# Kernel optimization log

Measured on AMD Instinct MI355X. Metric: run time of the kernel, lower is better.

## Reference

```python
import jax, jax.numpy as jnp
import numpy as np

QLEN, MLEN, BSZ = 1024, 1024, 8
D_MODEL, N_HEAD, D_HEAD = 512, 8, 64
KLEN = QLEN + MLEN
TAU = 1.0


def _rel_shift(x):
    # x: [qlen, klen, bsz, n_head] -- Transformer-XL relative shift
    q, k, b, n = x.shape
    zero_pad = jnp.zeros((q, 1, b, n), dtype=x.dtype)
    x_padded = jnp.concatenate([zero_pad, x], axis=1).reshape(k + 1, q, b, n)
    return x_padded[1:].reshape(q, k, b, n)


def setup_inputs() -> dict:
    key = jax.random.key(0)
    ks = jax.random.split(key, 8)
    w = jax.random.normal(ks[0], (QLEN, BSZ, D_MODEL), dtype=jnp.float32)
    r = jax.random.normal(ks[1], (KLEN, D_MODEL), dtype=jnp.float32)
    r_w_bias = jax.random.normal(ks[2], (N_HEAD, D_HEAD), dtype=jnp.float32) * 0.02
    r_r_bias = jax.random.normal(ks[3], (N_HEAD, D_HEAD), dtype=jnp.float32) * 0.02
    mems = jax.random.normal(ks[4], (MLEN, BSZ, D_MODEL), dtype=jnp.float32)
    W_qkv = jax.random.normal(ks[5], (D_MODEL, 3 * N_HEAD * D_HEAD), dtype=jnp.float32) * 0.02
    W_r = jax.random.normal(ks[6], (D_MODEL, N_HEAD * D_HEAD), dtype=jnp.float32) * 0.02
    W_o = jax.random.normal(ks[7], (N_HEAD * D_HEAD, D_MODEL), dtype=jnp.float32) * 0.02
    # causal mask with memory: query i can attend keys j <= i + MLEN
    i = jnp.arange(QLEN)[:, None]
    j = jnp.arange(KLEN)[None, :]
    attn_mask = (j > i + MLEN)[:, :, None]  # [qlen, klen, 1] bool, True = masked
    return {"w": w, "r": r, "r_w_bias": r_w_bias, "r_r_bias": r_r_bias,
            "mems": mems, "attn_mask": attn_mask,
            "W_qkv": W_qkv, "W_r": W_r, "W_o": W_o}


def reference(w, r, r_w_bias, r_r_bias, mems, attn_mask, W_qkv, W_r, W_o):
    qlen, bsz, d_model = w.shape
    n_head, d_head = r_w_bias.shape
    scale = 1.0 / np.sqrt(d_head).astype(np.float32)

    cat = jnp.concatenate([mems, w], axis=0)          # [klen, bsz, d_model]
    w_heads = cat @ W_qkv                              # [klen, bsz, 3*n*d]
    w_head_q, w_head_k, w_head_v = jnp.split(w_heads, 3, axis=-1)
    klen = w_head_k.shape[0]
    w_head_q = w_head_q[-qlen:].reshape(qlen, bsz, n_head, d_head)
    w_head_k = w_head_k.reshape(klen, bsz, n_head, d_head)
    w_head_v = w_head_v.reshape(klen, bsz, n_head, d_head)
    r_head_k = (r @ W_r).reshape(-1, n_head, d_head)   # [rlen, n, d]

    AC = jnp.einsum('ibnd,jbnd->ijbn', w_head_q + r_w_bias, w_head_k)
    BD = jnp.einsum('ibnd,jnd->ijbn', w_head_q + r_r_bias, r_head_k)
    BD = _rel_shift(BD)

    attn_score = (AC + BD) * scale                     # [q, k, b, n]
    mask4 = attn_mask[:, :, :, None]                   # [q, k, 1, 1]
    attn_score = jnp.where(mask4, -jnp.inf, attn_score)
    attn_prob = jax.nn.softmax(attn_score * TAU, axis=1)

    # attention entropy per head (no-grad in original)
    p_safe = jnp.where(mask4, 1.0, attn_prob)
    temp = -attn_prob * jnp.log(p_safe)
    attn_entropy = jax.lax.stop_gradient(jnp.mean(jnp.sum(temp, axis=1), axis=(0, 1)))  # [n_head]

    attn_vec = jnp.einsum('ijbn,jbnd->ibnd', attn_prob, w_head_v)
    attn_vec = attn_vec.reshape(qlen, bsz, n_head * d_head)
    attn_out = attn_vec @ W_o                          # [q, b, d_model]
    return attn_out, attn_entropy
```

## Files before the change

### kernel.cpp

```cpp
#include <hip/hip_runtime.h>
#include <hip/hip_bf16.h>


#define QLEN 1024
#define MLEN 1024
#define KLEN 2048
#define BSZ 8
#define DMODEL 512
#define NHEAD 8
#define DHEAD 64
#define SCALE 0.125f
#define RPAD 2176
#define RTHR 8.0f

#define B_QW   0u
#define B_QR   8388608u
#define B_K    16777216u
#define B_VT   33554432u
#define B_R    50331648u
#define B_AVB  52559872u
#define B_ENT  60948480u
#define B_ABF  60952576u
#define B_WQT  77729792u
#define B_RBF  79302656u
#define B_WRT  81399808u
#define B_WOT  81924096u

typedef short bf16x8 __attribute__((ext_vector_type(8)));
typedef float f32x4  __attribute__((ext_vector_type(4)));

#define SWZ(row, byte) ((((row) << 7) + (((((byte) >> 4) ^ ((row) & 7)) << 4)) + ((byte) & 15)))

__device__ __forceinline__ unsigned short f2bf(float f) {
    union { float f; unsigned int u; } v; v.f = f;
    unsigned int r = v.u + 0x7FFFu + ((v.u >> 16) & 1u);
    return (unsigned short)(r >> 16);
}

__global__ __launch_bounds__(256) void cvt_cat(const float* __restrict__ mems,
                                               const float* __restrict__ w,
                                               unsigned short* __restrict__ Abf) {
    size_t e = ((size_t)blockIdx.x * 256 + threadIdx.x) * 8;
    int m = (int)(e >> 9), k = (int)(e & 511);
    int t = m >> 3, b = m & 7;
    const float* src = (t < MLEN) ? mems + ((size_t)t * 8 + b) * 512 + k
                                  : w    + ((size_t)(t - MLEN) * 8 + b) * 512 + k;
    float4 v0 = *reinterpret_cast<const float4*>(src);
    float4 v1 = *reinterpret_cast<const float4*>(src + 4);
    ushort4 o0, o1;
    o0.x = f2bf(v0.x); o0.y = f2bf(v0.y); o0.z = f2bf(v0.z); o0.w = f2bf(v0.w);
    o1.x = f2bf(v1.x); o1.y = f2bf(v1.y); o1.z = f2bf(v1.z); o1.w = f2bf(v1.w);
    *reinterpret_cast<ushort4*>(Abf + e)     = o0;
    *reinterpret_cast<ushort4*>(Abf + e + 4) = o1;
}

__global__ __launch_bounds__(256) void cvt_r(const float* __restrict__ r,
                                             unsigned short* __restrict__ rbf) {
    size_t e = ((size_t)blockIdx.x * 256 + threadIdx.x) * 8;
    float4 v0 = *reinterpret_cast<const float4*>(r + e);
    float4 v1 = *reinterpret_cast<const float4*>(r + e + 4);
    ushort4 o0, o1;
    o0.x = f2bf(v0.x); o0.y = f2bf(v0.y); o0.z = f2bf(v0.z); o0.w = f2bf(v0.w);
    o1.x = f2bf(v1.x); o1.y = f2bf(v1.y); o1.z = f2bf(v1.z); o1.w = f2bf(v1.w);
    *reinterpret_cast<ushort4*>(rbf + e)     = o0;
    *reinterpret_cast<ushort4*>(rbf + e + 4) = o1;
}

__global__ __launch_bounds__(256) void tcvt(const float* __restrict__ S,
                                            unsigned short* __restrict__ D,
                                            int R, int C) {
    __shared__ float t[32][33];
    int bx = blockIdx.x * 32;
    int by = blockIdx.y * 32;
    int x = threadIdx.x & 31, y = threadIdx.x >> 5;
    #pragma unroll
    for (int q = 0; q < 4; ++q)
        t[y + q * 8][x] = S[(size_t)(by + y + q * 8) * C + bx + x];
    __syncthreads();
    #pragma unroll
    for (int q = 0; q < 4; ++q)
        D[(size_t)(bx + y + q * 8) * R + by + x] = f2bf(t[x][y + q * 8]);
}

__global__ void zpad_r(unsigned short* __restrict__ Rg) {
    int idx = blockIdx.x * 256 + threadIdx.x;
    int n = idx >> 10, o = idx & 1023;
    uint4 z = make_uint4(0, 0, 0, 0);
    *reinterpret_cast<uint4*>(Rg + ((size_t)n * RPAD + KLEN) * 64 + o * 8) = z;
}

template<int MODE>
__global__ __launch_bounds__(256) void gemm_mfma(const unsigned short* __restrict__ A,
                                                 const unsigned short* __restrict__ Bt,
                                                 const float* __restrict__ rwb,
                                                 const float* __restrict__ rrb,
                                                 unsigned short* __restrict__ QW,
                                                 unsigned short* __restrict__ QR,
                                                 unsigned short* __restrict__ Kg,
                                                 unsigned short* __restrict__ VT,
                                                 unsigned short* __restrict__ Rg,
                                                 float* __restrict__ Cout) {
    __shared__ unsigned short Als[128][72];
    __shared__ unsigned short Bls[128][72];
    const int tid = threadIdx.x;
    const int wv = tid >> 6, lane = tid & 63, lg = lane >> 4, lc = lane & 15;
    const int wr = wv >> 1, wc = wv & 1;
    const int n0 = blockIdx.x * 128;
    const int m0 = blockIdx.y * 128;

    f32x4 acc[4][4];
    #pragma unroll
    for (int mi = 0; mi < 4; ++mi)
        #pragma unroll
        for (int ni = 0; ni < 4; ++ni)
            acc[mi][ni] = (f32x4){0.f, 0.f, 0.f, 0.f};

    for (int k0 = 0; k0 < 512; k0 += 64) {
        __syncthreads();
        #pragma unroll
        for (int q = 0; q < 4; ++q) {
            int c = q * 256 + tid;
            int row = c >> 3, off = (c & 7) * 8;
            *reinterpret_cast<uint4*>(&Als[row][off]) =
                *reinterpret_cast<const uint4*>(A + (size_t)(m0 + row) * 512 + k0 + off);
            *reinterpret_cast<uint4*>(&Bls[row][off]) =
                *reinterpret_cast<const uint4*>(Bt + (size_t)(n0 + row) * 512 + k0 + off);
        }
        __syncthreads();
        #pragma unroll
        for (int kk = 0; kk < 2; ++kk) {
            bf16x8 af[4], bfr[4];
            #pragma unroll
            for (int mi = 0; mi < 4; ++mi)
                af[mi] = *reinterpret_cast<const bf16x8*>(&Als[64 * wr + 16 * mi + lc][32 * kk + lg * 8]);
            #pragma unroll
            for (int ni = 0; ni < 4; ++ni)
                bfr[ni] = *reinterpret_cast<const bf16x8*>(&Bls[64 * wc + 16 * ni + lc][32 * kk + lg * 8]);
            #pragma unroll
            for (int mi = 0; mi < 4; ++mi)
                #pragma unroll
                for (int ni = 0; ni < 4; ++ni)
                    acc[mi][ni] = __builtin_amdgcn_mfma_f32_16x16x32_bf16(af[mi], bfr[ni], acc[mi][ni], 0, 0, 0);
        }
    }

    #pragma unroll
    for (int mi = 0; mi < 4; ++mi) {
        #pragma unroll
        for (int ni = 0; ni < 4; ++ni) {
            const int n = n0 + 64 * wc + 16 * ni + lc;
            float bw = 0.f, br = 0.f;
            int region = 0, hn = 0, d = 0;
            if (MODE == 0) {
                region = n >> 9; int cr = n & 511; hn = cr >> 6; d = cr & 63;
                if (region == 0) { bw = rwb[hn * 64 + d]; br = rrb[hn * 64 + d]; }
            }
            #pragma unroll
            for (int reg = 0; reg < 4; ++reg) {
                const int m = m0 + 64 * wr + 16 * mi + lg * 4 + reg;
                const float val = acc[mi][ni][reg];
                if (MODE == 0) {
                    int t = m >> 3, b = m & 7, bn = b * 8 + hn;
                    if (region == 0) {
                        if (t >= MLEN) {
                            size_t base = ((size_t)bn * QLEN + (t - MLEN)) * 64 + d;
                            QW[base] = f2bf(val + bw);
                            QR[base] = f2bf(val + br);
                        }
                    } else if (region == 1) {
                        Kg[((size_t)bn * KLEN + t) * 64 + d] = f2bf(val);
                    } else {
                        VT[((size_t)bn * 64 + d) * KLEN + t] = f2bf(val);
                    }
                } else if (MODE == 1) {
                    Rg[((size_t)(n >> 6) * RPAD + m) * 64 + (n & 63)] = f2bf(val);
                } else {
                    Cout[(size_t)m * 512 + n] = val;
                }
            }
        }
    }
}

__global__ __launch_bounds__(256, 3) void attn_mfma(const unsigned short* __restrict__ QWg,
                                                    const unsigned short* __restrict__ QRg,
                                                    const unsigned short* __restrict__ Kg,
                                                    const unsigned short* __restrict__ VTg,
                                                    const unsigned short* __restrict__ Rg,
                                                    unsigned short* __restrict__ AVB,
                                                    float* __restrict__ ENT) {
    __shared__ __attribute__((aligned(16))) unsigned short Klds[64 * 64];
    __shared__ __attribute__((aligned(16))) unsigned short Rblds[128 * 64];
    __shared__ __attribute__((aligned(16))) unsigned short Vtlds[64 * 64];
    __shared__ __attribute__((aligned(16))) unsigned short Plds[64 * 64];

    const int tid = threadIdx.x;
    const int w = tid >> 6, lane = tid & 63, lg = lane >> 4, lc = lane & 15;
    const int iblk = ((blockIdx.y >> 4) & 1) ? (15 - blockIdx.x) : blockIdx.x;
    const int i0 = iblk * 64;
    const int bn = blockIdx.y, b = bn >> 3, n = bn & 7;
    const int srow = tid >> 3;
    const int sch  = tid & 7;

    {
        const unsigned short* qwsrc = QWg + ((size_t)bn * QLEN + i0) * 64;
        const unsigned short* qrsrc = QRg + ((size_t)bn * QLEN + i0) * 64;
        #pragma unroll
        for (int q = 0; q < 2; ++q) {
            int row = srow + q * 32;
            *reinterpret_cast<uint4*>((char*)Klds + SWZ(row, sch * 16)) =
                *reinterpret_cast<const uint4*>(qwsrc + (size_t)row * 64 + sch * 8);
            *reinterpret_cast<uint4*>((char*)Rblds + SWZ(row, sch * 16)) =
                *reinterpret_cast<const uint4*>(qrsrc + (size_t)row * 64 + sch * 8);
        }
    }
    __syncthreads();
    bf16x8 aqw[2], aqr[2];
    #pragma unroll
    for (int k = 0; k < 2; ++k) {
        aqw[k] = *reinterpret_cast<const bf16x8*>((const char*)Klds + SWZ(16 * w + lc, 64 * k + 16 * lg));
        aqr[k] = *reinterpret_cast<const bf16x8*>((const char*)Rblds + SWZ(16 * w + lc, 64 * k + 16 * lg));
    }

    f32x4 Ofr[4];
    #pragma unroll
    for (int t = 0; t < 4; ++t) Ofr[t] = (f32x4){0.f, 0.f, 0.f, 0.f};
    float mreg[4] = {-1e30f, -1e30f, -1e30f, -1e30f};
    float lpart[4] = {0.f, 0.f, 0.f, 0.f};
    float tpart[4] = {0.f, 0.f, 0.f, 0.f};

    const int nj = iblk + 17;
    const unsigned short* kbase = Kg  + (size_t)bn * KLEN * 64;
    const unsigned short* vbase = VTg + (size_t)bn * 64 * KLEN;
    const unsigned short* rbase = Rg  + (size_t)n * RPAD * 64 + (size_t)(960 - i0) * 64;

    uint4 kr0, kr1, vr0, vr1, rr0, rr1, rr2, rr3;
    kr0 = *reinterpret_cast<const uint4*>(kbase + (size_t)(srow)      * 64 + sch * 8);
    kr1 = *reinterpret_cast<const uint4*>(kbase + (size_t)(srow + 32) * 64 + sch * 8);
    vr0 = *reinterpret_cast<const uint4*>(vbase + (size_t)(srow)      * KLEN + sch * 8);
    vr1 = *reinterpret_cast<const uint4*>(vbase + (size_t)(srow + 32) * KLEN + sch * 8);
    rr0 = *reinterpret_cast<const uint4*>(rbase + (size_t)(srow)      * 64 + sch * 8);
    rr1 = *reinterpret_cast<const uint4*>(rbase + (size_t)(srow + 32) * 64 + sch * 8);
    rr2 = *reinterpret_cast<const uint4*>(rbase + (size_t)(srow + 64) * 64 + sch * 8);
    rr3 = *reinterpret_cast<const uint4*>(rbase + (size_t)(srow + 96) * 64 + sch * 8);

    for (int jt = 0; jt < nj; ++jt) {
        const int j0 = jt * 64;
        __syncthreads();

        *reinterpret_cast<uint4*>((char*)Klds  + SWZ(srow,      sch * 16)) = kr0;
        *reinterpret_cast<uint4*>((char*)Klds  + SWZ(srow + 32, sch * 16)) = kr1;
        *reinterpret_cast<uint4*>((char*)Vtlds + SWZ(srow,      sch * 16)) = vr0;
        *reinterpret_cast<uint4*>((char*)Vtlds + SWZ(srow + 32, sch * 16)) = vr1;
        *reinterpret_cast<uint4*>((char*)Rblds + SWZ(srow,      sch * 16)) = rr0;
        *reinterpret_cast<uint4*>((char*)Rblds + SWZ(srow + 32, sch * 16)) = rr1;
        *reinterpret_cast<uint4*>((char*)Rblds + SWZ(srow + 64, sch * 16)) = rr2;
        *reinterpret_cast<uint4*>((char*)Rblds + SWZ(srow + 96, sch * 16)) = rr3;

        if (jt + 1 < nj) {
            const int j1 = j0 + 64;
            kr0 = *reinterpret_cast<const uint4*>(kbase + (size_t)(j1 + srow)      * 64 + sch * 8);
            kr1 = *reinterpret_cast<const uint4*>(kbase + (size_t)(j1 + srow + 32) * 64 + sch * 8);
            vr0 = *reinterpret_cast<const uint4*>(vbase + (size_t)(srow)      * KLEN + j1 + sch * 8);
            vr1 = *reinterpret_cast<const uint4*>(vbase + (size_t)(srow + 32) * KLEN + j1 + sch * 8);
            rr0 = *reinterpret_cast<const uint4*>(rbase + (size_t)(j1 + srow)      * 64 + sch * 8);
            rr1 = *reinterpret_cast<const uint4*>(rbase + (size_t)(j1 + srow + 32) * 64 + sch * 8);
            rr2 = *reinterpret_cast<const uint4*>(rbase + (size_t)(j1 + srow + 64) * 64 + sch * 8);
            rr3 = *reinterpret_cast<const uint4*>(rbase + (size_t)(j1 + srow + 96) * 64 + sch * 8);
        }

        asm volatile("s_waitcnt lgkmcnt(0)" ::: "memory");
        __builtin_amdgcn_sched_barrier(0);
        __builtin_amdgcn_s_barrier();
        asm volatile("" ::: "memory");
        __builtin_amdgcn_sched_barrier(0);

        __builtin_amdgcn_s_setprio(1);
        f32x4 sfr[4];
        #pragma unroll
        for (int bj = 0; bj < 4; ++bj) {
            f32x4 acc = (f32x4){0.f, 0.f, 0.f, 0.f};
            #pragma unroll
            for (int k = 0; k < 2; ++k) {
                bf16x8 bk = *reinterpret_cast<const bf16x8*>((const char*)Klds + SWZ(16 * bj + lc, 64 * k + 16 * lg));
                acc = __builtin_amdgcn_mfma_f32_16x16x32_bf16(aqw[k], bk, acc, 0, 0, 0);
            }
            sfr[bj] = acc;
        }
        f32x4 g[5];
        const int sb = 48 - 16 * w;
        #pragma unroll
        for (int cb = 0; cb < 5; ++cb) {
            g[cb] = (f32x4){0.f, 0.f, 0.f, 0.f};
            #pragma unroll
            for (int k = 0; k < 2; ++k) {
                bf16x8 br = *reinterpret_cast<const bf16x8*>((const char*)Rblds + SWZ(sb + 16 * cb + lc, 64 * k + 16 * lg));
                g[cb] = __builtin_amdgcn_mfma_f32_16x16x32_bf16(aqr[k], br, g[cb], 0, 0, 0);
            }
        }
        __builtin_amdgcn_s_setprio(0);

        #pragma unroll
        for (int reg = 0; reg < 4; ++reg) {
            int r = lg * 4 + reg;
            int srcl = (lane & 48) | ((lc - r + 15) & 15);
            float gg[5];
            #pragma unroll
            for (int cb = 0; cb < 5; ++cb)
                gg[cb] = __shfl(g[cb][reg], srcl, 64);
            #pragma unroll
            for (int bj = 0; bj < 4; ++bj) {
                float gv = (lc <= r) ? gg[bj] : gg[bj + 1];
                sfr[bj][reg] = (sfr[bj][reg] + gv) * SCALE;
            }
        }
        if (jt == nj - 1) {
            #pragma unroll
            for (int bj = 0; bj < 4; ++bj)
                #pragma unroll
                for (int reg = 0; reg < 4; ++reg) {
                    int ii = 16 * w + lg * 4 + reg;
                    int jj = 16 * bj + lc;
                    if (j0 + jj > i0 + ii + MLEN) sfr[bj][reg] = -1e30f;
                }
        }

        float pm[4];
        #pragma unroll
        for (int reg = 0; reg < 4; ++reg)
            pm[reg] = fmaxf(fmaxf(sfr[0][reg], sfr[1][reg]), fmaxf(sfr[2][reg], sfr[3][reg]));
        bool grow = (pm[0] > mreg[0] + RTHR) || (pm[1] > mreg[1] + RTHR) ||
                    (pm[2] > mreg[2] + RTHR) || (pm[3] > mreg[3] + RTHR);
        if (__any(grow)) {
            #pragma unroll
            for (int reg = 0; reg < 4; ++reg) {
                float gmax = pm[reg];
                gmax = fmaxf(gmax, __shfl_xor(gmax, 1));
                gmax = fmaxf(gmax, __shfl_xor(gmax, 2));
                gmax = fmaxf(gmax, __shfl_xor(gmax, 4));
                gmax = fmaxf(gmax, __shfl_xor(gmax, 8));
                float mo = mreg[reg], mn = fmaxf(mo, gmax);
                float fac = __expf(mo - mn);
                lpart[reg] *= fac; tpart[reg] *= fac; mreg[reg] = mn;
                Ofr[0][reg] *= fac; Ofr[1][reg] *= fac;
                Ofr[2][reg] *= fac; Ofr[3][reg] *= fac;
            }
        }
        #pragma unroll
        for (int reg = 0; reg < 4; ++reg) {
            float mn = mreg[reg];
            float le = 0.f, te = 0.f;
            int r = lg * 4 + reg;
            #pragma unroll
            for (int bj = 0; bj < 4; ++bj) {
                float e = __expf(sfr[bj][reg] - mn);
                le += e; te += e * sfr[bj][reg];
                *reinterpret_cast<unsigned short*>((char*)Plds + SWZ(16 * w + r, 2 * (16 * bj + lc))) = f2bf(e);
            }
            lpart[reg] += le;
            tpart[reg] += te;
        }
        asm volatile("s_waitcnt lgkmcnt(0)" ::: "memory");
        __builtin_amdgcn_sched_barrier(0);

        __builtin_amdgcn_s_setprio(1);
        #pragma unroll
        for (int k = 0; k < 2; ++k) {
            bf16x8 ap = *reinterpret_cast<const bf16x8*>((const char*)Plds + SWZ(16 * w + lc, 64 * k + 16 * lg));
            Ofr[0] = __builtin_amdgcn_mfma_f32_16x16x32_bf16(ap,
                *reinterpret_cast<const bf16x8*>((const char*)Vtlds + SWZ( 0 + lc, 64 * k + 16 * lg)), Ofr[0], 0, 0, 0);
            Ofr[1] = __builtin_amdgcn_mfma_f32_16x16x32_bf16(ap,
                *reinterpret_cast<const bf16x8*>((const char*)Vtlds + SWZ(16 + lc, 64 * k + 16 * lg)), Ofr[1], 0, 0, 0);
            Ofr[2] = __builtin_amdgcn_mfma_f32_16x16x32_bf16(ap,
                *reinterpret_cast<const bf16x8*>((const char*)Vtlds + SWZ(32 + lc, 64 * k + 16 * lg)), Ofr[2], 0, 0, 0);
            Ofr[3] = __builtin_amdgcn_mfma_f32_16x16x32_bf16(ap,
                *reinterpret_cast<const bf16x8*>((const char*)Vtlds + SWZ(48 + lc, 64 * k + 16 * lg)), Ofr[3], 0, 0, 0);
        }
        __builtin_amdgcn_s_setprio(0);
    }

    float lred[4], tred[4];
    #pragma unroll
    for (int reg = 0; reg < 4; ++reg) {
        float l = lpart[reg], t = tpart[reg];
        l += __shfl_xor(l, 1); l += __shfl_xor(l, 2); l += __shfl_xor(l, 4); l += __shfl_xor(l, 8);
        t += __shfl_xor(t, 1); t += __shfl_xor(t, 2); t += __shfl_xor(t, 4); t += __shfl_xor(t, 8);
        lred[reg] = l; tred[reg] = t;
    }

    #pragma unroll
    for (int reg = 0; reg < 4; ++reg) {
        int i = i0 + 16 * w + lg * 4 + reg;
        float inv = 1.f / lred[reg];
        unsigned short* dst = AVB + ((size_t)i * BSZ + b) * DMODEL + n * 64 + lc;
        dst[ 0] = f2bf(Ofr[0][reg] * inv);
        dst[16] = f2bf(Ofr[1][reg] * inv);
        dst[32] = f2bf(Ofr[2][reg] * inv);
        dst[48] = f2bf(Ofr[3][reg] * inv);
    }

    float h = 0.f;
    if (lc == 0) {
        #pragma unroll
        for (int reg = 0; reg < 4; ++reg)
            h += mreg[reg] + __logf(lred[reg]) - tred[reg] / lred[reg];
    }
    h += __shfl_xor(h, 1);  h += __shfl_xor(h, 2);  h += __shfl_xor(h, 4);
    h += __shfl_xor(h, 8);  h += __shfl_xor(h, 16); h += __shfl_xor(h, 32);
    __syncthreads();
    float* hred = reinterpret_cast<float*>(Klds);
    if (lane == 0) hred[w] = h;
    __syncthreads();
    if (tid == 0) ENT[bn * 16 + iblk] = hred[0] + hred[1] + hred[2] + hred[3];
}

__global__ void reduce_ent(const float* __restrict__ ent, float* __restrict__ out) {
    int n = threadIdx.x;
    if (n < NHEAD) {
        float s = 0.f;
        for (int b = 0; b < BSZ; ++b)
            for (int it = 0; it < 16; ++it)
                s += ent[(b * NHEAD + n) * 16 + it];
        out[(size_t)QLEN * BSZ * DMODEL + n] = s / (float)(QLEN * BSZ);
    }
}

extern "C" void kernel_launch(void* const* d_in, const int* in_sizes, int n_in,
                              void* d_out, int out_size, void* d_ws, size_t ws_size,
                              hipStream_t stream) {
    const float* w    = (const float*)d_in[0];
    const float* r    = (const float*)d_in[1];
    const float* rwb  = (const float*)d_in[2];
    const float* rrb  = (const float*)d_in[3];
    const float* mems = (const float*)d_in[4];
    const float* Wqkv = (const float*)d_in[6];
    const float* Wr   = (const float*)d_in[7];
    const float* Wo   = (const float*)d_in[8];
    float* out = (float*)d_out;
    char*  wsb = (char*)d_ws;

    unsigned short* QW  = (unsigned short*)(wsb + B_QW);
    unsigned short* QR  = (unsigned short*)(wsb + B_QR);
    unsigned short* Kg  = (unsigned short*)(wsb + B_K);
    unsigned short* VT  = (unsigned short*)(wsb + B_VT);
    unsigned short* Rg  = (unsigned short*)(wsb + B_R);
    unsigned short* AVB = (unsigned short*)(wsb + B_AVB);
    float* ENT = (float*)(wsb + B_ENT);
    unsigned short* ABF = (unsigned short*)(wsb + B_ABF);
    unsigned short* WQT = (unsigned short*)(wsb + B_WQT);
    unsigned short* RBF = (unsigned short*)(wsb + B_RBF);
    unsigned short* WRT = (unsigned short*)(wsb + B_WRT);
    unsigned short* WOT = (unsigned short*)(wsb + B_WOT);

    cvt_cat<<<4096, 256, 0, stream>>>(mems, w, ABF);
    cvt_r<<<512, 256, 0, stream>>>(r, RBF);
    tcvt<<<dim3(48, 16), 256, 0, stream>>>(Wqkv, WQT, 512, 1536);
    tcvt<<<dim3(16, 16), 256, 0, stream>>>(Wr, WRT, 512, 512);
    tcvt<<<dim3(16, 16), 256, 0, stream>>>(Wo, WOT, 512, 512);
    zpad_r<<<32, 256, 0, stream>>>(Rg);

    gemm_mfma<0><<<dim3(12, 128), 256, 0, stream>>>(ABF, WQT, rwb, rrb, QW, QR, Kg, VT, nullptr, nullptr);
    gemm_mfma<1><<<dim3(4, 16), 256, 0, stream>>>(RBF, WRT, nullptr, nullptr,
                                                  nullptr, nullptr, nullptr, nullptr, Rg, nullptr);

    attn_mfma<<<dim3(16, 64), 256, 0, stream>>>(QW, QR, Kg, VT, Rg, AVB, ENT);
    reduce_ent<<<1, 64, 0, stream>>>(ENT, out);

    gemm_mfma<2><<<dim3(4, 64), 256, 0, stream>>>(AVB, WOT, nullptr, nullptr,
                                                  nullptr, nullptr, nullptr, nullptr, nullptr, out);
}
```

Before: 257.4 us.

## Double attention query tile to 128 rows with 8 warps per block

Each attention block now covers 128 query rows with 512 threads (8 waves) instead of 64 rows with 256 threads. The K, V and R tiles staged in LDS are shared by twice as many query rows, and the R window grows to 192 rows. The aim is to halve global and LDS traffic for K/V/R per query. In exchange the grid has half as many blocks (512), LDS use per block is larger, and the causal mask must now cover the last two key tiles.

```diff
diff --git a/kernel.cpp b/kernel.cpp
--- a/kernel.cpp
+++ b/kernel.cpp
@@ -182,7 +182,7 @@
     }
 }
 
-__global__ __launch_bounds__(256, 3) void attn_mfma(const unsigned short* __restrict__ QWg,
+__global__ __launch_bounds__(512, 4) void attn_mfma(const unsigned short* __restrict__ QWg,
                                                     const unsigned short* __restrict__ QRg,
                                                     const unsigned short* __restrict__ Kg,
                                                     const unsigned short* __restrict__ VTg,
@@ -190,14 +190,14 @@
                                                     unsigned short* __restrict__ AVB,
                                                     float* __restrict__ ENT) {
     __shared__ __attribute__((aligned(16))) unsigned short Klds[64 * 64];
-    __shared__ __attribute__((aligned(16))) unsigned short Rblds[128 * 64];
+    __shared__ __attribute__((aligned(16))) unsigned short Rblds[192 * 64];
     __shared__ __attribute__((aligned(16))) unsigned short Vtlds[64 * 64];
-    __shared__ __attribute__((aligned(16))) unsigned short Plds[64 * 64];
+    __shared__ __attribute__((aligned(16))) unsigned short Plds[128 * 64];
 
     const int tid = threadIdx.x;
     const int w = tid >> 6, lane = tid & 63, lg = lane >> 4, lc = lane & 15;
-    const int iblk = ((blockIdx.y >> 4) & 1) ? (15 - blockIdx.x) : blockIdx.x;
-    const int i0 = iblk * 64;
+    const int iblk = ((blockIdx.y >> 5) & 1) ? (7 - blockIdx.x) : blockIdx.x;
+    const int i0 = iblk * 128;
     const int bn = blockIdx.y, b = bn >> 3, n = bn & 7;
     const int srow = tid >> 3;
     const int sch  = tid & 7;
@@ -207,10 +207,10 @@
         const unsigned short* qrsrc = QRg + ((size_t)bn * QLEN + i0) * 64;
         #pragma unroll
         for (int q = 0; q < 2; ++q) {
-            int row = srow + q * 32;
-            *reinterpret_cast<uint4*>((char*)Klds + SWZ(row, sch * 16)) =
+            int row = srow + q * 64;
+            *reinterpret_cast<uint4*>((char*)Rblds + SWZ(row, sch * 16)) =
                 *reinterpret_cast<const uint4*>(qwsrc + (size_t)row * 64 + sch * 8);
-            *reinterpret_cast<uint4*>((char*)Rblds + SWZ(row, sch * 16)) =
+            *reinterpret_cast<uint4*>((char*)Plds + SWZ(row, sch * 16)) =
                 *reinterpret_cast<const uint4*>(qrsrc + (size_t)row * 64 + sch * 8);
         }
     }
@@ -218,8 +218,8 @@
     bf16x8 aqw[2], aqr[2];
     #pragma unroll
     for (int k = 0; k < 2; ++k) {
-        aqw[k] = *reinterpret_cast<const bf16x8*>((const char*)Klds + SWZ(16 * w + lc, 64 * k + 16 * lg));
-        aqr[k] = *reinterpret_cast<const bf16x8*>((const char*)Rblds + SWZ(16 * w + lc, 64 * k + 16 * lg));
+        aqw[k] = *reinterpret_cast<const bf16x8*>((const char*)Rblds + SWZ(16 * w + lc, 64 * k + 16 * lg));
+        aqr[k] = *reinterpret_cast<const bf16x8*>((const char*)Plds + SWZ(16 * w + lc, 64 * k + 16 * lg));
     }
 
     f32x4 Ofr[4];
@@ -229,44 +229,35 @@
     float lpart[4] = {0.f, 0.f, 0.f, 0.f};
     float tpart[4] = {0.f, 0.f, 0.f, 0.f};
 
-    const int nj = iblk + 17;
+    const int nj = 2 * iblk + 18;
     const unsigned short* kbase = Kg  + (size_t)bn * KLEN * 64;
     const unsigned short* vbase = VTg + (size_t)bn * 64 * KLEN;
-    const unsigned short* rbase = Rg  + (size_t)n * RPAD * 64 + (size_t)(960 - i0) * 64;
-
-    uint4 kr0, kr1, vr0, vr1, rr0, rr1, rr2, rr3;
-    kr0 = *reinterpret_cast<const uint4*>(kbase + (size_t)(srow)      * 64 + sch * 8);
-    kr1 = *reinterpret_cast<const uint4*>(kbase + (size_t)(srow + 32) * 64 + sch * 8);
-    vr0 = *reinterpret_cast<const uint4*>(vbase + (size_t)(srow)      * KLEN + sch * 8);
-    vr1 = *reinterpret_cast<const uint4*>(vbase + (size_t)(srow + 32) * KLEN + sch * 8);
-    rr0 = *reinterpret_cast<const uint4*>(rbase + (size_t)(srow)      * 64 + sch * 8);
-    rr1 = *reinterpret_cast<const uint4*>(rbase + (size_t)(srow + 32) * 64 + sch * 8);
-    rr2 = *reinterpret_cast<const uint4*>(rbase + (size_t)(srow + 64) * 64 + sch * 8);
-    rr3 = *reinterpret_cast<const uint4*>(rbase + (size_t)(srow + 96) * 64 + sch * 8);
+    const unsigned short* rbase = Rg  + (size_t)n * RPAD * 64 + (size_t)(896 - i0) * 64;
+
+    uint4 kr0, vr0, rr0, rr1, rr2;
+    kr0 = *reinterpret_cast<const uint4*>(kbase + (size_t)srow * 64 + sch * 8);
+    vr0 = *reinterpret_cast<const uint4*>(vbase + (size_t)srow * KLEN + sch * 8);
+    rr0 = *reinterpret_cast<const uint4*>(rbase + (size_t)(srow)       * 64 + sch * 8);
+    rr1 = *reinterpret_cast<const uint4*>(rbase + (size_t)(srow + 64)  * 64 + sch * 8);
+    rr2 = *reinterpret_cast<const uint4*>(rbase + (size_t)(srow + 128) * 64 + sch * 8);
 
     for (int jt = 0; jt < nj; ++jt) {
         const int j0 = jt * 64;
         __syncthreads();
 
-        *reinterpret_cast<uint4*>((char*)Klds  + SWZ(srow,      sch * 16)) = kr0;
-        *reinterpret_cast<uint4*>((char*)Klds  + SWZ(srow + 32, sch * 16)) = kr1;
-        *reinterpret_cast<uint4*>((char*)Vtlds + SWZ(srow,      sch * 16)) = vr0;
-        *reinterpret_cast<uint4*>((char*)Vtlds + SWZ(srow + 32, sch * 16)) = vr1;
-        *reinterpret_cast<uint4*>((char*)Rblds + SWZ(srow,      sch * 16)) = rr0;
-        *reinterpret_cast<uint4*>((char*)Rblds + SWZ(srow + 32, sch * 16)) = rr1;
-        *reinterpret_cast<uint4*>((char*)Rblds + SWZ(srow + 64, sch * 16)) = rr2;
-        *reinterpret_cast<uint4*>((char*)Rblds + SWZ(srow + 96, sch * 16)) = rr3;
+        *reinterpret_cast<uint4*>((char*)Klds  + SWZ(srow,       sch * 16)) = kr0;
+        *reinterpret_cast<uint4*>((char*)Vtlds + SWZ(srow,       sch * 16)) = vr0;
+        *reinterpret_cast<uint4*>((char*)Rblds + SWZ(srow,       sch * 16)) = rr0;
+        *reinterpret_cast<uint4*>((char*)Rblds + SWZ(srow + 64,  sch * 16)) = rr1;
+        *reinterpret_cast<uint4*>((char*)Rblds + SWZ(srow + 128, sch * 16)) = rr2;
 
         if (jt + 1 < nj) {
             const int j1 = j0 + 64;
-            kr0 = *reinterpret_cast<const uint4*>(kbase + (size_t)(j1 + srow)      * 64 + sch * 8);
-            kr1 = *reinterpret_cast<const uint4*>(kbase + (size_t)(j1 + srow + 32) * 64 + sch * 8);
-            vr0 = *reinterpret_cast<const uint4*>(vbase + (size_t)(srow)      * KLEN + j1 + sch * 8);
-            vr1 = *reinterpret_cast<const uint4*>(vbase + (size_t)(srow + 32) * KLEN + j1 + sch * 8);
-            rr0 = *reinterpret_cast<const uint4*>(rbase + (size_t)(j1 + srow)      * 64 + sch * 8);
-            rr1 = *reinterpret_cast<const uint4*>(rbase + (size_t)(j1 + srow + 32) * 64 + sch * 8);
-            rr2 = *reinterpret_cast<const uint4*>(rbase + (size_t)(j1 + srow + 64) * 64 + sch * 8);
-            rr3 = *reinterpret_cast<const uint4*>(rbase + (size_t)(j1 + srow + 96) * 64 + sch * 8);
+            kr0 = *reinterpret_cast<const uint4*>(kbase + (size_t)(j1 + srow) * 64 + sch * 8);
+            vr0 = *reinterpret_cast<const uint4*>(vbase + (size_t)srow * KLEN + j1 + sch * 8);
+            rr0 = *reinterpret_cast<const uint4*>(rbase + (size_t)(j1 + srow)       * 64 + sch * 8);
+            rr1 = *reinterpret_cast<const uint4*>(rbase + (size_t)(j1 + srow + 64)  * 64 + sch * 8);
+            rr2 = *reinterpret_cast<const uint4*>(rbase + (size_t)(j1 + srow + 128) * 64 + sch * 8);
         }
 
         asm volatile("s_waitcnt lgkmcnt(0)" ::: "memory");
@@ -288,7 +279,7 @@
             sfr[bj] = acc;
         }
         f32x4 g[5];
-        const int sb = 48 - 16 * w;
+        const int sb = 112 - 16 * w;
         #pragma unroll
         for (int cb = 0; cb < 5; ++cb) {
             g[cb] = (f32x4){0.f, 0.f, 0.f, 0.f};
@@ -314,7 +305,7 @@
                 sfr[bj][reg] = (sfr[bj][reg] + gv) * SCALE;
             }
         }
-        if (jt == nj - 1) {
+        if (jt >= nj - 2) {
             #pragma unroll
             for (int bj = 0; bj < 4; ++bj)
                 #pragma unroll
@@ -411,7 +402,12 @@
     float* hred = reinterpret_cast<float*>(Klds);
     if (lane == 0) hred[w] = h;
     __syncthreads();
-    if (tid == 0) ENT[bn * 16 + iblk] = hred[0] + hred[1] + hred[2] + hred[3];
+    if (tid == 0) {
+        float s = 0.f;
+        #pragma unroll
+        for (int q = 0; q < 8; ++q) s += hred[q];
+        ENT[bn * 8 + iblk] = s;
+    }
 }
 
 __global__ void reduce_ent(const float* __restrict__ ent, float* __restrict__ out) {
@@ -419,8 +415,8 @@
     if (n < NHEAD) {
         float s = 0.f;
         for (int b = 0; b < BSZ; ++b)
-            for (int it = 0; it < 16; ++it)
-                s += ent[(b * NHEAD + n) * 16 + it];
+            for (int it = 0; it < 8; ++it)
+                s += ent[(b * NHEAD + n) * 8 + it];
         out[(size_t)QLEN * BSZ * DMODEL + n] = s / (float)(QLEN * BSZ);
     }
 }
@@ -463,7 +459,7 @@
     gemm_mfma<1><<<dim3(4, 16), 256, 0, stream>>>(RBF, WRT, nullptr, nullptr,
                                                   nullptr, nullptr, nullptr, nullptr, Rg, nullptr);
 
-    attn_mfma<<<dim3(16, 64), 256, 0, stream>>>(QW, QR, Kg, VT, Rg, AVB, ENT);
+    attn_mfma<<<dim3(8, 64), 512, 0, stream>>>(QW, QR, Kg, VT, Rg, AVB, ENT);
     reduce_ent<<<1, 64, 0, stream>>>(ENT, out);
 
     gemm_mfma<2><<<dim3(4, 64), 256, 0, stream>>>(AVB, WOT, nullptr, nullptr,
```

Result: slower. 376.5 us (+46.3%).
